# Kernel optimization log

Hardware: AMD Instinct MI355X
Metric: run time of the kernel (lower is better)

## Reference

```python
import jax, jax.numpy as jnp
import numpy as np

B, NNODE, FIN, FOUT = 64, 512, 64, 64

def setup_inputs() -> dict:
    key = jax.random.key(0)
    ks = jax.random.split(key, 8)
    stdW = 1.0 / np.sqrt(FIN)
    stdA = 1.0 / np.sqrt(FOUT)
    return {
        "X": jax.random.normal(ks[0], (B, NNODE, FIN), dtype=jnp.float32),
        "A": jax.random.uniform(ks[1], (B, NNODE, NNODE), dtype=jnp.float32),
        "N": jax.random.randint(ks[2], (B,), 1, NNODE + 1, dtype=jnp.int64),
        "W": jax.random.uniform(ks[3], (FIN, FOUT), jnp.float32, -stdW, stdW),
        "a": jax.random.uniform(ks[4], (FOUT, FOUT), jnp.float32, -stdA, stdA),
        "bias_W": jax.random.uniform(ks[5], (FOUT,), jnp.float32, -stdW, stdW),
        "bias_a": jax.random.uniform(ks[6], (NNODE,), jnp.float32, -1.0 / np.sqrt(NNODE), 1.0 / np.sqrt(NNODE)),
    }

def reference(X, A, N, W, a, bias_W, bias_a):
    # A_ = A + identity on the top-left n_atoms block (only diagonal entries)
    idx = jnp.arange(A.shape[1])
    diag_mask = (idx[None, :] < N[:, None]).astype(A.dtype)  # [B, n]
    A_ = A + jnp.einsum('bn,nm->bnm', diag_mask, jnp.eye(A.shape[1], dtype=A.dtype))
    # XW: [B, n, F_out]
    XW = jnp.einsum('bnc,cd->bnd', X, W)
    # buf[a,j,k] = sum_i a[i,j] * XW^T[a,j,k]  (einsum 'ij,ajk->ajk')
    col_sum = a.sum(axis=0)  # [F_out]
    XWT = jnp.swapaxes(XW, 1, 2)  # [B, F_out, n]
    buf = col_sum[None, :, None] * XWT
    Z = jnp.einsum('bif,bfk->bik', XW, buf) + bias_a  # [B, n, n] + [n] broadcast on last dim
    att = jnp.tanh(jnp.einsum('bij,bjk->bik', A_, Z))
    H = jnp.einsum('bij,bjd->bid', att, XW) + bias_W
    return H
```

## Files before the change

### kernel.cpp

```cpp
#include <hip/hip_runtime.h>

#define BB 64
#define NN 512
#define FD 64

typedef short bf16x8 __attribute__((ext_vector_type(8)));
typedef float f32x4 __attribute__((ext_vector_type(4)));

__device__ __forceinline__ unsigned short f2bf(float f){
    unsigned u = __builtin_bit_cast(unsigned, f);
    u += 0x7fffu + ((u >> 16) & 1u);
    return (unsigned short)(u >> 16);
}
__device__ __forceinline__ float bf2f(unsigned short h){
    unsigned u = ((unsigned)h) << 16;
    return __builtin_bit_cast(float, u);
}
__device__ __forceinline__ float fast_tanh(float x){
    float e = __expf(2.0f * x);
    return 1.0f - 2.0f * __builtin_amdgcn_rcpf(e + 1.0f);
}

__global__ __launch_bounds__(256) void k_prep(const float* __restrict__ W,
                                              const float* __restrict__ a,
                                              float* __restrict__ colsum,
                                              unsigned short* __restrict__ Wt){
    __shared__ float Wl[64][68];
    __shared__ float cpart[4][64];
    int t = threadIdx.x;
    int d = t & 63, part = t >> 6;
    float s = 0.f;
    #pragma unroll
    for (int i = 0; i < 16; i++) s += a[(part*16 + i)*64 + d];
    cpart[part][d] = s;
    int r = t >> 2, c0 = (t & 3) * 16;
    {
        const float4* src = (const float4*)&W[r*64 + c0];
        #pragma unroll
        for (int q = 0; q < 4; q++) *(float4*)&Wl[r][c0 + q*4] = src[q];
    }
    __syncthreads();
    if (part == 0) colsum[d] = cpart[0][d] + cpart[1][d] + cpart[2][d] + cpart[3][d];
    #pragma unroll
    for (int q = 0; q < 4; q++){
        ushort4 o;
        #pragma unroll
        for (int jj = 0; jj < 4; jj++)
            ((unsigned short*)&o)[jj] = f2bf(Wl[c0 + q*4 + jj][r]);
        *(ushort4*)&Wt[r*64 + c0 + q*4] = o;
    }
}

__global__ __launch_bounds__(256) void k_xw(const float* __restrict__ X,
                                            const unsigned short* __restrict__ Wt,
                                            unsigned short* __restrict__ XWh,
                                            unsigned short* __restrict__ XWt){
    __shared__ unsigned short Xl[64][72];
    __shared__ unsigned short Wtl[64][72];
    __shared__ unsigned short Cl[64][72];
    __shared__ unsigned short ClT[64][72];
    int t = threadIdx.x;
    int row0 = blockIdx.x * 64;
    int r = t >> 2, c0 = (t & 3) * 16;
    {
        const float4* src = (const float4*)&X[(row0 + r)*FD + c0];
        #pragma unroll
        for (int q = 0; q < 4; q++){
            float4 v = src[q];
            ushort4 h; h.x=f2bf(v.x); h.y=f2bf(v.y); h.z=f2bf(v.z); h.w=f2bf(v.w);
            *(ushort4*)&Xl[r][c0 + q*4] = h;
        }
        const uint4* src2 = (const uint4*)&Wt[r*64 + c0];
        *(uint4*)&Wtl[r][c0]     = src2[0];
        *(uint4*)&Wtl[r][c0 + 8] = src2[1];
    }
    __syncthreads();
    int lane = t & 63, w = t >> 6, l15 = lane & 15, quad = lane >> 4;
    f32x4 acc[4] = {{0,0,0,0},{0,0,0,0},{0,0,0,0},{0,0,0,0}};
    #pragma unroll
    for (int ks = 0; ks < 2; ks++){
        bf16x8 af = *(const bf16x8*)&Xl[w*16 + l15][ks*32 + quad*8];
        #pragma unroll
        for (int nt = 0; nt < 4; nt++){
            bf16x8 bfr = *(const bf16x8*)&Wtl[nt*16 + l15][ks*32 + quad*8];
            acc[nt] = __builtin_amdgcn_mfma_f32_16x16x32_bf16(af, bfr, acc[nt], 0, 0, 0);
        }
    }
    #pragma unroll
    for (int nt = 0; nt < 4; nt++)
        #pragma unroll
        for (int rg = 0; rg < 4; rg++){
            unsigned short hb = f2bf(acc[nt][rg]);
            Cl [w*16 + quad*4 + rg][nt*16 + l15] = hb;
            ClT[nt*16 + l15][w*16 + quad*4 + rg] = hb;
        }
    __syncthreads();
    int b = blockIdx.x >> 3, n0 = (blockIdx.x & 7) * 64;
    {
        uint4 v0 = *(const uint4*)&Cl[r][c0];
        uint4 v1 = *(const uint4*)&Cl[r][c0 + 8];
        *(uint4*)&XWh[(row0 + r)*FD + c0]     = v0;
        *(uint4*)&XWh[(row0 + r)*FD + c0 + 8] = v1;
    }
    {
        uint4 v0 = *(const uint4*)&ClT[r][c0];
        uint4 v1 = *(const uint4*)&ClT[r][c0 + 8];
        *(uint4*)&XWt[(b*64 + r)*NN + n0 + c0]     = v0;
        *(uint4*)&XWt[(b*64 + r)*NN + n0 + c0 + 8] = v1;
    }
}

__global__ __launch_bounds__(512) void k_fused(const float* __restrict__ A,
                                               const unsigned short* __restrict__ XWh,
                                               const unsigned short* __restrict__ XWt,
                                               const float* __restrict__ colsum,
                                               const int* __restrict__ Ni,
                                               const float* __restrict__ bias_a,
                                               const float* __restrict__ bias_W,
                                               float* __restrict__ H){
    __shared__ unsigned short s0[64][72];
    __shared__ unsigned short s1[64][72];
    __shared__ unsigned short MPl[64][72];
    __shared__ float rspart[64][8];
    __shared__ float rsl[64];
    __shared__ float csl[64];
    __shared__ float bl[64];
    int t = threadIdx.x;
    int b = blockIdx.y, it = blockIdx.x;
    int i0 = it * 64;
    int Nb = (Ni[1] == 0) ? Ni[2*b] : Ni[b];
    int r8 = t >> 3, c4 = (t & 7) * 4, c8 = (t & 7) * 8;
    int lane = t & 63, w = t >> 6, l15 = lane & 15, quad = lane >> 4;
    int wr = w & 3, wc = w >> 2;
    if (t < 64) csl[t] = colsum[t];
    const float* Ab = A + (b*NN + i0)*NN;

    float4 pA0, pA1; uint4 pB;
    pA0 = *(const float4*)&Ab[r8*NN + c4];
    pA1 = *(const float4*)&Ab[r8*NN + 32 + c4];
    pB  = *(const uint4*)&XWt[(b*64 + r8)*NN + c8];
    f32x4 acc[2] = {{0,0,0,0},{0,0,0,0}};
    float rs = 0.f;
    for (int c = 0; c < 8; c++){
        __syncthreads();
        {
            float4 v = pA0;
            rs += v.x + v.y + v.z + v.w;
            ushort4 h; h.x=f2bf(v.x); h.y=f2bf(v.y); h.z=f2bf(v.z); h.w=f2bf(v.w);
            *(ushort4*)&s0[r8][c4] = h;
            v = pA1;
            rs += v.x + v.y + v.z + v.w;
            ushort4 h2; h2.x=f2bf(v.x); h2.y=f2bf(v.y); h2.z=f2bf(v.z); h2.w=f2bf(v.w);
            *(ushort4*)&s0[r8][32 + c4] = h2;
        }
        *(uint4*)&s1[r8][c8] = pB;
        __syncthreads();
        if (c < 7){
            pA0 = *(const float4*)&Ab[r8*NN + (c+1)*64 + c4];
            pA1 = *(const float4*)&Ab[r8*NN + (c+1)*64 + 32 + c4];
            pB  = *(const uint4*)&XWt[(b*64 + r8)*NN + (c+1)*64 + c8];
        }
        #pragma unroll
        for (int ks = 0; ks < 2; ks++){
            bf16x8 af = *(const bf16x8*)&s0[wr*16 + l15][ks*32 + quad*8];
            #pragma unroll
            for (int nt = 0; nt < 2; nt++){
                bf16x8 bfr = *(const bf16x8*)&s1[wc*32 + nt*16 + l15][ks*32 + quad*8];
                acc[nt] = __builtin_amdgcn_mfma_f32_16x16x32_bf16(af, bfr, acc[nt], 0, 0, 0);
            }
        }
        if (c == it){
            #pragma unroll
            for (int nt = 0; nt < 2; nt++)
                #pragma unroll
                for (int rg = 0; rg < 4; rg++){
                    int iloc = wr*16 + quad*4 + rg;
                    if (i0 + iloc < Nb)
                        acc[nt][rg] += bf2f(s1[wc*32 + nt*16 + l15][iloc]);
                }
        }
    }
    rspart[r8][t & 7] = rs;
    #pragma unroll
    for (int nt = 0; nt < 2; nt++){
        float cs = csl[wc*32 + nt*16 + l15];
        #pragma unroll
        for (int rg = 0; rg < 4; rg++)
            MPl[wr*16 + quad*4 + rg][wc*32 + nt*16 + l15] = f2bf(acc[nt][rg] * cs);
    }
    __syncthreads();
    if (t < 64){
        float s = 0.f;
        #pragma unroll
        for (int p = 0; p < 8; p++) s += rspart[t][p];
        if (i0 + t < Nb) s += 1.f;
        rsl[t] = s;
    }
    __syncthreads();
    bf16x8 maf[2];
    maf[0] = *(const bf16x8*)&MPl[wr*16 + l15][quad*8];
    maf[1] = *(const bf16x8*)&MPl[wr*16 + l15][32 + quad*8];
    float rs_r[4];
    #pragma unroll
    for (int rg = 0; rg < 4; rg++) rs_r[rg] = rsl[wr*16 + quad*4 + rg];

    uint4 q1, q2;
    q1 = *(const uint4*)&XWh[(b*NN + r8)*FD + c8];
    q2 = *(const uint4*)&XWt[(b*64 + r8)*NN + c8];
    f32x4 hacc[2] = {{0,0,0,0},{0,0,0,0}};
    for (int jt = 0; jt < 8; jt++){
        __syncthreads();
        *(uint4*)&s0[r8][c8] = q1;
        *(uint4*)&s1[r8][c8] = q2;
        if (t < 64) bl[t] = bias_a[jt*64 + t];
        __syncthreads();
        if (jt < 7){
            q1 = *(const uint4*)&XWh[(b*NN + (jt+1)*64 + r8)*FD + c8];
            q2 = *(const uint4*)&XWt[(b*64 + r8)*NN + (jt+1)*64 + c8];
        }
        #pragma unroll
        for (int nt = 0; nt < 2; nt++){
            float bv = bl[wc*32 + nt*16 + l15];
            f32x4 arg = { rs_r[0]*bv, rs_r[1]*bv, rs_r[2]*bv, rs_r[3]*bv };
            #pragma unroll
            for (int ks = 0; ks < 2; ks++){
                bf16x8 bfr = *(const bf16x8*)&s0[wc*32 + nt*16 + l15][ks*32 + quad*8];
                arg = __builtin_amdgcn_mfma_f32_16x16x32_bf16(maf[ks], bfr, arg, 0, 0, 0);
            }
            #pragma unroll
            for (int rg = 0; rg < 4; rg++)
                MPl[wr*16 + quad*4 + rg][wc*32 + nt*16 + l15] = f2bf(fast_tanh(arg[rg]));
        }
        __syncthreads();
        #pragma unroll
        for (int ks = 0; ks < 2; ks++){
            bf16x8 paf = *(const bf16x8*)&MPl[wr*16 + l15][ks*32 + quad*8];
            #pragma unroll
            for (int dt = 0; dt < 2; dt++){
                bf16x8 bfr = *(const bf16x8*)&s1[wc*32 + dt*16 + l15][ks*32 + quad*8];
                hacc[dt] = __builtin_amdgcn_mfma_f32_16x16x32_bf16(paf, bfr, hacc[dt], 0, 0, 0);
            }
        }
    }
    #pragma unroll
    for (int dt = 0; dt < 2; dt++){
        float bw = bias_W[wc*32 + dt*16 + l15];
        #pragma unroll
        for (int rg = 0; rg < 4; rg++)
            H[(b*NN + i0 + wr*16 + quad*4 + rg)*FD + wc*32 + dt*16 + l15] = hacc[dt][rg] + bw;
    }
}

extern "C" void kernel_launch(void* const* d_in, const int* in_sizes, int n_in,
                              void* d_out, int out_size, void* d_ws, size_t ws_size,
                              hipStream_t stream){
    const float* X      = (const float*)d_in[0];
    const float* A      = (const float*)d_in[1];
    const int*   N      = (const int*)  d_in[2];
    const float* W      = (const float*)d_in[3];
    const float* a      = (const float*)d_in[4];
    const float* bias_W = (const float*)d_in[5];
    const float* bias_a = (const float*)d_in[6];
    float* H = (float*)d_out;
    char* ws = (char*)d_ws;

    unsigned short* XWh    = (unsigned short*)(ws);
    unsigned short* XWt    = (unsigned short*)(ws + (4u<<20));
    unsigned short* Wt     = (unsigned short*)(ws + (8u<<20));
    float*          colsum = (float*)(ws + (8u<<20) + 8192);

    k_prep <<<1, 256, 0, stream>>>(W, a, colsum, Wt);
    k_xw   <<<BB * NN / 64, 256, 0, stream>>>(X, Wt, XWh, XWt);
    k_fused<<<dim3(8, BB), 512, 0, stream>>>(A, XWh, XWt, colsum, N, bias_a, bias_W, H);
}
```

Baseline: 130.6 us.

## Remove prep kernel and halve fused row tile to double block count

After: 138.0 us. +5.7%, slower.

```diff
diff --git a/kernel.cpp b/kernel.cpp
--- a/kernel.cpp
+++ b/kernel.cpp
@@ -21,38 +21,8 @@
     return 1.0f - 2.0f * __builtin_amdgcn_rcpf(e + 1.0f);
 }
 
-__global__ __launch_bounds__(256) void k_prep(const float* __restrict__ W,
-                                              const float* __restrict__ a,
-                                              float* __restrict__ colsum,
-                                              unsigned short* __restrict__ Wt){
-    __shared__ float Wl[64][68];
-    __shared__ float cpart[4][64];
-    int t = threadIdx.x;
-    int d = t & 63, part = t >> 6;
-    float s = 0.f;
-    #pragma unroll
-    for (int i = 0; i < 16; i++) s += a[(part*16 + i)*64 + d];
-    cpart[part][d] = s;
-    int r = t >> 2, c0 = (t & 3) * 16;
-    {
-        const float4* src = (const float4*)&W[r*64 + c0];
-        #pragma unroll
-        for (int q = 0; q < 4; q++) *(float4*)&Wl[r][c0 + q*4] = src[q];
-    }
-    __syncthreads();
-    if (part == 0) colsum[d] = cpart[0][d] + cpart[1][d] + cpart[2][d] + cpart[3][d];
-    #pragma unroll
-    for (int q = 0; q < 4; q++){
-        ushort4 o;
-        #pragma unroll
-        for (int jj = 0; jj < 4; jj++)
-            ((unsigned short*)&o)[jj] = f2bf(Wl[c0 + q*4 + jj][r]);
-        *(ushort4*)&Wt[r*64 + c0 + q*4] = o;
-    }
-}
-
 __global__ __launch_bounds__(256) void k_xw(const float* __restrict__ X,
-                                            const unsigned short* __restrict__ Wt,
+                                            const float* __restrict__ W,
                                             unsigned short* __restrict__ XWh,
                                             unsigned short* __restrict__ XWt){
     __shared__ unsigned short Xl[64][72];
@@ -63,6 +33,15 @@
     int row0 = blockIdx.x * 64;
     int r = t >> 2, c0 = (t & 3) * 16;
     {
+        const float4* wsrc = (const float4*)&W[r*64 + c0];
+        #pragma unroll
+        for (int q = 0; q < 4; q++){
+            float4 v = wsrc[q];
+            Wtl[c0 + q*4 + 0][r] = f2bf(v.x);
+            Wtl[c0 + q*4 + 1][r] = f2bf(v.y);
+            Wtl[c0 + q*4 + 2][r] = f2bf(v.z);
+            Wtl[c0 + q*4 + 3][r] = f2bf(v.w);
+        }
         const float4* src = (const float4*)&X[(row0 + r)*FD + c0];
         #pragma unroll
         for (int q = 0; q < 4; q++){
@@ -70,9 +49,6 @@
             ushort4 h; h.x=f2bf(v.x); h.y=f2bf(v.y); h.z=f2bf(v.z); h.w=f2bf(v.w);
             *(ushort4*)&Xl[r][c0 + q*4] = h;
         }
-        const uint4* src2 = (const uint4*)&Wt[r*64 + c0];
-        *(uint4*)&Wtl[r][c0]     = src2[0];
-        *(uint4*)&Wtl[r][c0 + 8] = src2[1];
     }
     __syncthreads();
     int lane = t & 63, w = t >> 6, l15 = lane & 15, quad = lane >> 4;
@@ -110,91 +86,98 @@
     }
 }
 
-__global__ __launch_bounds__(512) void k_fused(const float* __restrict__ A,
-                                               const unsigned short* __restrict__ XWh,
-                                               const unsigned short* __restrict__ XWt,
-                                               const float* __restrict__ colsum,
-                                               const int* __restrict__ Ni,
-                                               const float* __restrict__ bias_a,
-                                               const float* __restrict__ bias_W,
-                                               float* __restrict__ H){
+__global__ __launch_bounds__(512, 8) void k_fused(const float* __restrict__ A,
+                                                  const unsigned short* __restrict__ XWh,
+                                                  const unsigned short* __restrict__ XWt,
+                                                  const float* __restrict__ a,
+                                                  const int* __restrict__ Ni,
+                                                  const float* __restrict__ bias_a,
+                                                  const float* __restrict__ bias_W,
+                                                  float* __restrict__ H){
     __shared__ unsigned short s0[64][72];
     __shared__ unsigned short s1[64][72];
-    __shared__ unsigned short MPl[64][72];
-    __shared__ float rspart[64][8];
-    __shared__ float rsl[64];
+    __shared__ unsigned short MPl[32][72];
+    __shared__ float cspart[8][64];
     __shared__ float csl[64];
-    __shared__ float bl[64];
+    __shared__ float rspart[32][16];
+    __shared__ float rsl[32];
+    __shared__ float bl[512];
     int t = threadIdx.x;
     int b = blockIdx.y, it = blockIdx.x;
-    int i0 = it * 64;
+    int i0 = it * 32;
     int Nb = (Ni[1] == 0) ? Ni[2*b] : Ni[b];
-    int r8 = t >> 3, c4 = (t & 7) * 4, c8 = (t & 7) * 8;
     int lane = t & 63, w = t >> 6, l15 = lane & 15, quad = lane >> 4;
-    int wr = w & 3, wc = w >> 2;
-    if (t < 64) csl[t] = colsum[t];
+    int wr = w & 1, wc = w >> 1;
+    int r16 = t >> 4, cA = (t & 15) * 4;
+    int r8 = t >> 3, c8 = (t & 7) * 8;
     const float* Ab = A + (b*NN + i0)*NN;
-
-    float4 pA0, pA1; uint4 pB;
-    pA0 = *(const float4*)&Ab[r8*NN + c4];
-    pA1 = *(const float4*)&Ab[r8*NN + 32 + c4];
-    pB  = *(const uint4*)&XWt[(b*64 + r8)*NN + c8];
-    f32x4 acc[2] = {{0,0,0,0},{0,0,0,0}};
+    const unsigned short* XWtb = XWt + b*64*NN;
+    const unsigned short* XWhb = XWh + b*NN*FD;
+
+    {
+        int cd = t & 63, cp = t >> 6;
+        float s = 0.f;
+        #pragma unroll
+        for (int i = 0; i < 8; i++) s += a[(cp*8 + i)*64 + cd];
+        cspart[cp][cd] = s;
+    }
+    bl[t] = bias_a[t];
+
+    float4 pA = *(const float4*)&Ab[r16*NN + cA];
+    uint4  pB = *(const uint4*)&XWtb[r8*NN + c8];
+    f32x4 acc = {0,0,0,0};
     float rs = 0.f;
+    int diagc = it >> 1;
     for (int c = 0; c < 8; c++){
         __syncthreads();
         {
-            float4 v = pA0;
+            float4 v = pA;
             rs += v.x + v.y + v.z + v.w;
             ushort4 h; h.x=f2bf(v.x); h.y=f2bf(v.y); h.z=f2bf(v.z); h.w=f2bf(v.w);
-            *(ushort4*)&s0[r8][c4] = h;
-            v = pA1;
-            rs += v.x + v.y + v.z + v.w;
-            ushort4 h2; h2.x=f2bf(v.x); h2.y=f2bf(v.y); h2.z=f2bf(v.z); h2.w=f2bf(v.w);
-            *(ushort4*)&s0[r8][32 + c4] = h2;
+            *(ushort4*)&s0[r16][cA] = h;
         }
         *(uint4*)&s1[r8][c8] = pB;
         __syncthreads();
         if (c < 7){
-            pA0 = *(const float4*)&Ab[r8*NN + (c+1)*64 + c4];
-            pA1 = *(const float4*)&Ab[r8*NN + (c+1)*64 + 32 + c4];
-            pB  = *(const uint4*)&XWt[(b*64 + r8)*NN + (c+1)*64 + c8];
+            pA = *(const float4*)&Ab[r16*NN + (c+1)*64 + cA];
+            pB = *(const uint4*)&XWtb[r8*NN + (c+1)*64 + c8];
         }
         #pragma unroll
         for (int ks = 0; ks < 2; ks++){
-            bf16x8 af = *(const bf16x8*)&s0[wr*16 + l15][ks*32 + quad*8];
+            bf16x8 af  = *(const bf16x8*)&s0[wr*16 + l15][ks*32 + quad*8];
+            bf16x8 bfr = *(const bf16x8*)&s1[wc*16 + l15][ks*32 + quad*8];
+            acc = __builtin_amdgcn_mfma_f32_16x16x32_bf16(af, bfr, acc, 0, 0, 0);
+        }
+        if (c == diagc){
             #pragma unroll
-            for (int nt = 0; nt < 2; nt++){
-                bf16x8 bfr = *(const bf16x8*)&s1[wc*32 + nt*16 + l15][ks*32 + quad*8];
-                acc[nt] = __builtin_amdgcn_mfma_f32_16x16x32_bf16(af, bfr, acc[nt], 0, 0, 0);
+            for (int rg = 0; rg < 4; rg++){
+                int li = wr*16 + quad*4 + rg;
+                if (i0 + li < Nb)
+                    acc[rg] += bf2f(s1[wc*16 + l15][(it & 1)*32 + li]);
             }
         }
-        if (c == it){
-            #pragma unroll
-            for (int nt = 0; nt < 2; nt++)
-                #pragma unroll
-                for (int rg = 0; rg < 4; rg++){
-                    int iloc = wr*16 + quad*4 + rg;
-                    if (i0 + iloc < Nb)
-                        acc[nt][rg] += bf2f(s1[wc*32 + nt*16 + l15][iloc]);
-                }
-        }
-    }
-    rspart[r8][t & 7] = rs;
-    #pragma unroll
-    for (int nt = 0; nt < 2; nt++){
-        float cs = csl[wc*32 + nt*16 + l15];
-        #pragma unroll
-        for (int rg = 0; rg < 4; rg++)
-            MPl[wr*16 + quad*4 + rg][wc*32 + nt*16 + l15] = f2bf(acc[nt][rg] * cs);
-    }
+    }
+    rspart[r16][t & 15] = rs;
     __syncthreads();
     if (t < 64){
         float s = 0.f;
         #pragma unroll
-        for (int p = 0; p < 8; p++) s += rspart[t][p];
-        if (i0 + t < Nb) s += 1.f;
-        rsl[t] = s;
+        for (int p = 0; p < 8; p++) s += cspart[p][t];
+        csl[t] = s;
+    } else if (t < 96){
+        int row = t - 64;
+        float s = 0.f;
+        #pragma unroll
+        for (int p = 0; p < 16; p++) s += rspart[row][p];
+        if (i0 + row < Nb) s += 1.f;
+        rsl[row] = s;
+    }
+    __syncthreads();
+    {
+        float cs = csl[wc*16 + l15];
+        #pragma unroll
+        for (int rg = 0; rg < 4; rg++)
+            MPl[wr*16 + quad*4 + rg][wc*16 + l15] = f2bf(acc[rg] * cs);
     }
     __syncthreads();
     bf16x8 maf[2];
@@ -204,50 +187,43 @@
     #pragma unroll
     for (int rg = 0; rg < 4; rg++) rs_r[rg] = rsl[wr*16 + quad*4 + rg];
 
-    uint4 q1, q2;
-    q1 = *(const uint4*)&XWh[(b*NN + r8)*FD + c8];
-    q2 = *(const uint4*)&XWt[(b*64 + r8)*NN + c8];
-    f32x4 hacc[2] = {{0,0,0,0},{0,0,0,0}};
+    uint4 q1 = *(const uint4*)&XWhb[r8*FD + c8];
+    uint4 q2 = *(const uint4*)&XWtb[r8*NN + c8];
+    f32x4 hacc = {0,0,0,0};
     for (int jt = 0; jt < 8; jt++){
         __syncthreads();
         *(uint4*)&s0[r8][c8] = q1;
         *(uint4*)&s1[r8][c8] = q2;
-        if (t < 64) bl[t] = bias_a[jt*64 + t];
         __syncthreads();
         if (jt < 7){
-            q1 = *(const uint4*)&XWh[(b*NN + (jt+1)*64 + r8)*FD + c8];
-            q2 = *(const uint4*)&XWt[(b*64 + r8)*NN + (jt+1)*64 + c8];
-        }
-        #pragma unroll
-        for (int nt = 0; nt < 2; nt++){
-            float bv = bl[wc*32 + nt*16 + l15];
+            q1 = *(const uint4*)&XWhb[((jt+1)*64 + r8)*FD + c8];
+            q2 = *(const uint4*)&XWtb[r8*NN + (jt+1)*64 + c8];
+        }
+        {
+            float bv = bl[jt*64 + wc*16 + l15];
             f32x4 arg = { rs_r[0]*bv, rs_r[1]*bv, rs_r[2]*bv, rs_r[3]*bv };
             #pragma unroll
             for (int ks = 0; ks < 2; ks++){
-                bf16x8 bfr = *(const bf16x8*)&s0[wc*32 + nt*16 + l15][ks*32 + quad*8];
+                bf16x8 bfr = *(const bf16x8*)&s0[wc*16 + l15][ks*32 + quad*8];
                 arg = __builtin_amdgcn_mfma_f32_16x16x32_bf16(maf[ks], bfr, arg, 0, 0, 0);
             }
             #pragma unroll
             for (int rg = 0; rg < 4; rg++)
-                MPl[wr*16 + quad*4 + rg][wc*32 + nt*16 + l15] = f2bf(fast_tanh(arg[rg]));
+                MPl[wr*16 + quad*4 + rg][wc*16 + l15] = f2bf(fast_tanh(arg[rg]));
         }
         __syncthreads();
         #pragma unroll
         for (int ks = 0; ks < 2; ks++){
             bf16x8 paf = *(const bf16x8*)&MPl[wr*16 + l15][ks*32 + quad*8];
-            #pragma unroll
-            for (int dt = 0; dt < 2; dt++){
-                bf16x8 bfr = *(const bf16x8*)&s1[wc*32 + dt*16 + l15][ks*32 + quad*8];
-                hacc[dt] = __builtin_amdgcn_mfma_f32_16x16x32_bf16(paf, bfr, hacc[dt], 0, 0, 0);
-            }
-        }
-    }
-    #pragma unroll
-    for (int dt = 0; dt < 2; dt++){
-        float bw = bias_W[wc*32 + dt*16 + l15];
+            bf16x8 bfr = *(const bf16x8*)&s1[wc*16 + l15][ks*32 + quad*8];
+            hacc = __builtin_amdgcn_mfma_f32_16x16x32_bf16(paf, bfr, hacc, 0, 0, 0);
+        }
+    }
+    {
+        float bw = bias_W[wc*16 + l15];
         #pragma unroll
         for (int rg = 0; rg < 4; rg++)
-            H[(b*NN + i0 + wr*16 + quad*4 + rg)*FD + wc*32 + dt*16 + l15] = hacc[dt][rg] + bw;
+            H[(b*NN + i0 + wr*16 + quad*4 + rg)*FD + wc*16 + l15] = hacc[rg] + bw;
     }
 }
 
@@ -264,12 +240,9 @@
     float* H = (float*)d_out;
     char* ws = (char*)d_ws;
 
-    unsigned short* XWh    = (unsigned short*)(ws);
-    unsigned short* XWt    = (unsigned short*)(ws + (4u<<20));
-    unsigned short* Wt     = (unsigned short*)(ws + (8u<<20));
-    float*          colsum = (float*)(ws + (8u<<20) + 8192);
-
-    k_prep <<<1, 256, 0, stream>>>(W, a, colsum, Wt);
-    k_xw   <<<BB * NN / 64, 256, 0, stream>>>(X, Wt, XWh, XWt);
-    k_fused<<<dim3(8, BB), 512, 0, stream>>>(A, XWh, XWt, colsum, N, bias_a, bias_W, H);
-}
+    unsigned short* XWh = (unsigned short*)(ws);
+    unsigned short* XWt = (unsigned short*)(ws + (4u<<20));
+
+    k_xw   <<<BB * NN / 64, 256, 0, stream>>>(X, W, XWh, XWt);
+    k_fused<<<dim3(16, BB), 512, 0, stream>>>(A, XWh, XWt, a, N, bias_a, bias_W, H);
+}
```
